# Optimization experiments

Measured on AMD Instinct MI355X. Metric: run time of the kernel, lower is better.

Reference implementation:

```python
import jax, jax.numpy as jnp
import numpy as np

B = 2
Z, Y, X = 21, 256, 256          # spatial_shape (z, y, x)
OZ, OY, OX = 10, 128, 128       # strided conv output grid: floor((in+2p-3)/2)+1
CIN, C1, C2 = 16, 32, 64
N = 400_000
EPS = 1e-3                      # BN eps from norm_cfg


def setup_inputs() -> dict:
    rng = np.random.default_rng(0)
    total = B * Z * Y * X
    lin = rng.choice(total, size=N, replace=False)
    lin.sort()
    b = (lin // (Z * Y * X)).astype(np.int64)
    r = lin % (Z * Y * X)
    z = r // (Y * X)
    r = r % (Y * X)
    y = r // X
    x = r % X
    coors = np.stack([b, z, y, x], axis=1).astype(np.int32)

    # Active output coords of SparseConv3d(k=3, s=2, pad=[0,1,1]):
    # input c is seen by output o iff o*2 - p + j == c for some j in {0,1,2}.
    pads = (0, 1, 1)
    cand_dims = []
    for c, p, osz in zip((z, y, x), pads, (OZ, OY, OX)):
        per = []
        for j in range(3):
            num = c + p - j
            o = num // 2
            valid = (num % 2 == 0) & (num >= 0) & (o < osz)
            per.append((o, valid))
        cand_dims.append(per)
    cand = []
    for oz, vz in cand_dims[0]:
        for oy, vy in cand_dims[1]:
            for ox, vx in cand_dims[2]:
                v = vz & vy & vx
                if v.any():
                    cand.append(np.stack([b[v], oz[v], oy[v], ox[v]], axis=1))
    out_coors = np.unique(np.concatenate(cand, axis=0), axis=0).astype(np.int32)

    key = jax.random.key(0)
    ks = jax.random.split(key, 11)
    voxel_feat = jax.random.normal(ks[0], (N, CIN), jnp.float32)
    W1 = jax.random.normal(ks[1], (27, CIN, C1), jnp.float32) / np.float32(np.sqrt(27 * CIN))
    W2 = jax.random.normal(ks[2], (27, C1, C2), jnp.float32) / np.float32(np.sqrt(27 * C1))
    g1 = 1.0 + 0.1 * jax.random.normal(ks[3], (C1,), jnp.float32)
    b1 = 0.1 * jax.random.normal(ks[4], (C1,), jnp.float32)
    m1 = 0.1 * jax.random.normal(ks[5], (C1,), jnp.float32)
    v1 = 0.5 + jnp.abs(jax.random.normal(ks[6], (C1,), jnp.float32)) * 0.5
    g2 = 1.0 + 0.1 * jax.random.normal(ks[7], (C2,), jnp.float32)
    b2 = 0.1 * jax.random.normal(ks[8], (C2,), jnp.float32)
    m2 = 0.1 * jax.random.normal(ks[9], (C2,), jnp.float32)
    v2 = 0.5 + jnp.abs(jax.random.normal(ks[10], (C2,), jnp.float32)) * 0.5
    return {
        "voxel_feat": voxel_feat,
        "coors": jnp.asarray(coors),
        "out_coors": jnp.asarray(out_coors),
        "W1": W1, "g1": g1, "b1": b1, "m1": m1, "v1": v1,
        "W2": W2, "g2": g2, "b2": b2, "m2": m2, "v2": v2,
        "batch_size": B,
    }


def _bn_relu(x, g, b, m, v):
    return jax.nn.relu((x - m) * (g * jax.lax.rsqrt(v + EPS)) + b)


def _build_grid(coors, n):
    # dense hash of active voxels -> row index (rulebook lookup table)
    lin = ((coors[:, 0] * Z + coors[:, 1]) * Y + coors[:, 2]) * X + coors[:, 3]
    return jnp.full((B * Z * Y * X,), -1, jnp.int32).at[lin].set(jnp.arange(n, dtype=jnp.int32))


def _sparse_conv(feat, grid, bcol, zz, yy, xx, W, cout):
    # gather-GEMM-scatter for one kernel offset set; loop over 27 offsets is structural
    n = zz[0].shape[0]
    out = jnp.zeros((n, cout), feat.dtype)
    for k in range(27):
        z_, y_, x_ = zz[k], yy[k], xx[k]
        ok = (z_ >= 0) & (z_ < Z) & (y_ >= 0) & (y_ < Y) & (x_ >= 0) & (x_ < X)
        l = ((bcol * Z + jnp.clip(z_, 0, Z - 1)) * Y + jnp.clip(y_, 0, Y - 1)) * X + jnp.clip(x_, 0, X - 1)
        idx = grid[l]
        ok = ok & (idx >= 0)
        f = feat[jnp.where(ok, idx, 0)]
        out = out + jnp.where(ok[:, None], f @ W[k], jnp.zeros((), feat.dtype))
    return out


def reference(voxel_feat, coors, out_coors, W1, g1, b1, m1, v1, W2, g2, b2, m2, v2, batch_size):
    n = voxel_feat.shape[0]
    grid = _build_grid(coors, n)

    # --- SubMConv3d(k=3, pad=1): out[c] = sum_j W1[j] @ in[c + j - 1], outputs only at input sites
    zz, yy, xx = [], [], []
    for dz in (-1, 0, 1):
        for dy in (-1, 0, 1):
            for dx in (-1, 0, 1):
                zz.append(coors[:, 1] + dz)
                yy.append(coors[:, 2] + dy)
                xx.append(coors[:, 3] + dx)
    f1 = _bn_relu(_sparse_conv(voxel_feat, grid, coors[:, 0], zz, yy, xx, W1, C1), g1, b1, m1, v1)

    # --- SparseConv3d(k=3, s=2, pad=[0,1,1]): input coord = o*2 - p + j
    zz, yy, xx = [], [], []
    for jz in range(3):
        for jy in range(3):
            for jx in range(3):
                zz.append(out_coors[:, 1] * 2 - 0 + jz)
                yy.append(out_coors[:, 2] * 2 - 1 + jy)
                xx.append(out_coors[:, 3] * 2 - 1 + jx)
    f2 = _bn_relu(_sparse_conv(f1, grid, out_coors[:, 0], zz, yy, xx, W2, C2), g2, b2, m2, v2)

    return f2, out_coors, batch_size
```

## Files before the change

kernel.cpp:

```cpp
#include <hip/hip_runtime.h>

#define ZD 21
#define YD 256
#define XD 256
#define BD 2
#define NCIN 16
#define NC1 32
#define NC2 64
#define BN_EPS 1e-3f

#define ZP 23
#define YP 258
#define XP 258
#define YPXP 66564
#define GRID_TOT (BD * ZP * YPXP)
#define TAILN 133647

typedef __attribute__((ext_vector_type(8))) short short8;
typedef __attribute__((ext_vector_type(4))) float floatx4;

__constant__ int KOFF[28] = {
    0, 1, 2, 258, 259, 260, 516, 517, 518,
    66564, 66565, 66566, 66822, 66823, 66824, 67080, 67081, 67082,
    133128, 133129, 133130, 133386, 133387, 133388, 133644, 133645, 133646,
    0};

__device__ inline unsigned short rne_bf16(float w) {
    unsigned b = __float_as_uint(w);
    return (unsigned short)((b + 0x7FFFu + ((b >> 16) & 1u)) >> 16);
}

__global__ __launch_bounds__(256) void scatter_grid_k(const int* __restrict__ coors,
                                                      int* __restrict__ grid, int n) {
    int i = blockIdx.x * 256 + threadIdx.x;
    if (i >= n) return;
    const int4 c = ((const int4*)coors)[i];
    const int lin = ((c.x * ZP + c.y + 1) * YP + c.z + 1) * XP + c.w + 1;
    grid[lin] = i;
}

__global__ __launch_bounds__(256) void feat2bf_k(const float* __restrict__ feat,
                                                 unsigned short* __restrict__ fb, int n8) {
    int i = blockIdx.x * 256 + threadIdx.x;
    if (i >= n8) return;
    const float4* p = (const float4*)feat + (size_t)i * 2;
    const float4 a = p[0], b = p[1];
    short8 o;
    o[0] = (short)rne_bf16(a.x); o[1] = (short)rne_bf16(a.y);
    o[2] = (short)rne_bf16(a.z); o[3] = (short)rne_bf16(a.w);
    o[4] = (short)rne_bf16(b.x); o[5] = (short)rne_bf16(b.y);
    o[6] = (short)rne_bf16(b.z); o[7] = (short)rne_bf16(b.w);
    ((short8*)fb)[i] = o;
}

__global__ __launch_bounds__(256) void pack_w_k(const float* __restrict__ W1,
                                                const float* __restrict__ W2,
                                                short* __restrict__ wp1,
                                                short* __restrict__ wp2) {
    int t = blockIdx.x * 256 + threadIdx.x;
    if (t < 14 * 2 * 512) {
        int pair = t / 1024, r = t % 1024, cb = r / 512, e = r % 512;
        int lane = e / 8, j = e % 8, kk = (lane >> 4) * 8 + j;
        int ko = pair * 2 + (kk >> 4), ci = kk & 15, co = cb * 16 + (lane & 15);
        float w = (ko < 27) ? W1[(ko * NCIN + ci) * NC1 + co] : 0.f;
        wp1[(pair * 2 + cb) * 512 + e] = (short)rne_bf16(w);
    }
    int t2 = t - 14 * 2 * 512;
    if (t2 >= 0 && t2 < 27 * 4 * 512) {
        int k = t2 / 2048, r = t2 % 2048, cb = r / 512, e = r % 512;
        int lane = e / 8, j = e % 8, ci = (lane >> 4) * 8 + j, co = cb * 16 + (lane & 15);
        wp2[(k * 4 + cb) * 512 + e] = (short)rne_bf16(W2[(k * NC1 + ci) * NC2 + co]);
    }
}

__global__ __launch_bounds__(256, 4) void conv1_k(
    const unsigned short* __restrict__ featb, const int* __restrict__ coors,
    const short* __restrict__ wp1,
    const float* __restrict__ g1, const float* __restrict__ b1,
    const float* __restrict__ m1, const float* __restrict__ v1,
    const int* __restrict__ gridp, unsigned short* __restrict__ f1, int n, int tail0) {
    const int tid = threadIdx.x;
    const int lane = tid & 63;
    const int quad = lane >> 4;
    const int mrow = lane & 15;
    const int vbase = blockIdx.x * 256 + (tid >> 6) * 64;
    const int ko_add = quad >> 1;
    const int ci_half = quad & 1;

    int pb[4];
#pragma unroll
    for (int mt = 0; mt < 4; ++mt) {
        const int v = vbase + mt * 16 + mrow;
        if (v < n) {
            const int4 cc = ((const int4*)coors)[v];
            pb[mt] = ((cc.x * ZP + cc.y) * YP + cc.z) * XP + cc.w;
        } else {
            pb[mt] = tail0;
        }
    }

    floatx4 d[4][2];
#pragma unroll
    for (int mt = 0; mt < 4; ++mt)
#pragma unroll
        for (int cb = 0; cb < 2; ++cb) d[mt][cb] = (floatx4){0.f, 0.f, 0.f, 0.f};

    const short8* __restrict__ wb = (const short8*)wp1;

    int id_c[4], id_n[4];
    {
        const int koff = ko_add ? KOFF[1] : KOFF[0];
#pragma unroll
        for (int mt = 0; mt < 4; ++mt) id_c[mt] = gridp[pb[mt] + koff];
    }
    {
        const int koff = ko_add ? KOFF[3] : KOFF[2];
#pragma unroll
        for (int mt = 0; mt < 4; ++mt) id_n[mt] = gridp[pb[mt] + koff];
    }
    short8 a_c[4];
#pragma unroll
    for (int mt = 0; mt < 4; ++mt) {
        a_c[mt] = (short8)0;
        if (id_c[mt] >= 0)
            a_c[mt] = *(const short8*)(featb + (unsigned)(id_c[mt] * NCIN + ci_half * 8));
    }
    short8 w0_c = wb[0 * 64 + lane];
    short8 w1_c = wb[1 * 64 + lane];

#pragma unroll 2
    for (int pair = 0; pair < 14; ++pair) {
        unsigned long long bm[4];
#pragma unroll
        for (int mt = 0; mt < 4; ++mt) bm[mt] = __ballot(id_c[mt] >= 0);

        short8 a_nx[4];
#pragma unroll
        for (int mt = 0; mt < 4; ++mt) {
            a_nx[mt] = (short8)0;
            if (id_n[mt] >= 0)
                a_nx[mt] = *(const short8*)(featb + (unsigned)(id_n[mt] * NCIN + ci_half * 8));
        }
        int id_f[4];
        {
            const int kbase = (pair < 12) ? (pair + 2) * 2 : 26;
            const int koff = ko_add ? KOFF[kbase + 1] : KOFF[kbase];
#pragma unroll
            for (int mt = 0; mt < 4; ++mt) id_f[mt] = gridp[pb[mt] + koff];
        }
        const int kn = (pair < 13) ? pair + 1 : 13;
        const short8 w0_n = wb[(kn * 2 + 0) * 64 + lane];
        const short8 w1_n = wb[(kn * 2 + 1) * 64 + lane];

#pragma unroll
        for (int mt = 0; mt < 4; ++mt) {
            if (bm[mt]) {
                d[mt][0] = __builtin_amdgcn_mfma_f32_16x16x32_bf16(a_c[mt], w0_c, d[mt][0], 0, 0, 0);
                d[mt][1] = __builtin_amdgcn_mfma_f32_16x16x32_bf16(a_c[mt], w1_c, d[mt][1], 0, 0, 0);
            }
        }
#pragma unroll
        for (int mt = 0; mt < 4; ++mt) {
            a_c[mt] = a_nx[mt]; id_c[mt] = id_n[mt]; id_n[mt] = id_f[mt];
        }
        w0_c = w0_n; w1_c = w1_n;
    }

    const int col = lane & 15;
#pragma unroll
    for (int cb = 0; cb < 2; ++cb) {
        const int ch = cb * 16 + col;
        const float sc = g1[ch] * rsqrtf(v1[ch] + BN_EPS);
        const float sb = b1[ch] - m1[ch] * sc;
#pragma unroll
        for (int mt = 0; mt < 4; ++mt) {
#pragma unroll
            for (int r = 0; r < 4; ++r) {
                const int v = vbase + mt * 16 + quad * 4 + r;
                if (v < n) {
                    const float o = fmaxf(fmaf(d[mt][cb][r], sc, sb), 0.f);
                    f1[(unsigned)(v * NC1 + ch)] = rne_bf16(o);
                }
            }
        }
    }
}

__global__ __launch_bounds__(256, 3) void conv2_k(
    const unsigned short* __restrict__ f1,
    const int* __restrict__ ocoors, const short* __restrict__ wp2,
    const float* __restrict__ g2, const float* __restrict__ b2,
    const float* __restrict__ m2, const float* __restrict__ v2,
    const int* __restrict__ gridp, float* __restrict__ out, int m, int tail0) {
    const int tid = threadIdx.x;
    const int lane = tid & 63;
    const int quad = lane >> 4;
    const int mrow = lane & 15;
    const int vbase = blockIdx.x * 256 + (tid >> 6) * 64;

    int pb[4];
#pragma unroll
    for (int mt = 0; mt < 4; ++mt) {
        const int v = vbase + mt * 16 + mrow;
        if (v < m) {
            const int4 cc = ((const int4*)ocoors)[v];
            pb[mt] = ((cc.x * ZP + 2 * cc.y + 1) * YP + 2 * cc.z) * XP + 2 * cc.w;
        } else {
            pb[mt] = tail0;
        }
    }

    floatx4 d[4][4];
#pragma unroll
    for (int mt = 0; mt < 4; ++mt)
#pragma unroll
        for (int cb = 0; cb < 4; ++cb) d[mt][cb] = (floatx4){0.f, 0.f, 0.f, 0.f};

    const short8* __restrict__ wb = (const short8*)wp2;

    int id_c[4], id_n[4];
#pragma unroll
    for (int mt = 0; mt < 4; ++mt) id_c[mt] = gridp[pb[mt] + KOFF[0]];
#pragma unroll
    for (int mt = 0; mt < 4; ++mt) id_n[mt] = gridp[pb[mt] + KOFF[1]];
    short8 a_c[4];
#pragma unroll
    for (int mt = 0; mt < 4; ++mt) {
        a_c[mt] = (short8)0;
        if (id_c[mt] >= 0)
            a_c[mt] = *(const short8*)(f1 + (unsigned)(id_c[mt] * NC1 + quad * 8));
    }
    short8 w_c[4];
#pragma unroll
    for (int cb = 0; cb < 4; ++cb) w_c[cb] = wb[(0 * 4 + cb) * 64 + lane];

#pragma unroll 2
    for (int k = 0; k < 27; ++k) {
        unsigned long long bm[4];
#pragma unroll
        for (int mt = 0; mt < 4; ++mt) bm[mt] = __ballot(id_c[mt] >= 0);

        short8 a_nx[4];
#pragma unroll
        for (int mt = 0; mt < 4; ++mt) {
            a_nx[mt] = (short8)0;
            if (id_n[mt] >= 0)
                a_nx[mt] = *(const short8*)(f1 + (unsigned)(id_n[mt] * NC1 + quad * 8));
        }
        int id_f[4];
        {
            const int koff = KOFF[(k < 25) ? k + 2 : 26];
#pragma unroll
            for (int mt = 0; mt < 4; ++mt) id_f[mt] = gridp[pb[mt] + koff];
        }
        const int kn = (k < 26) ? k + 1 : 26;
        short8 w_n[4];
#pragma unroll
        for (int cb = 0; cb < 4; ++cb) w_n[cb] = wb[(kn * 4 + cb) * 64 + lane];

#pragma unroll
        for (int mt = 0; mt < 4; ++mt) {
            if (bm[mt]) {
#pragma unroll
                for (int cb = 0; cb < 4; ++cb)
                    d[mt][cb] = __builtin_amdgcn_mfma_f32_16x16x32_bf16(a_c[mt], w_c[cb], d[mt][cb], 0, 0, 0);
            }
        }
#pragma unroll
        for (int mt = 0; mt < 4; ++mt) {
            a_c[mt] = a_nx[mt]; id_c[mt] = id_n[mt]; id_n[mt] = id_f[mt];
        }
#pragma unroll
        for (int cb = 0; cb < 4; ++cb) w_c[cb] = w_n[cb];
    }

    const int col = lane & 15;
#pragma unroll
    for (int cb = 0; cb < 4; ++cb) {
        const int ch = cb * 16 + col;
        const float sc = g2[ch] * rsqrtf(v2[ch] + BN_EPS);
        const float sb = b2[ch] - m2[ch] * sc;
#pragma unroll
        for (int mt = 0; mt < 4; ++mt) {
#pragma unroll
            for (int r = 0; r < 4; ++r) {
                const int v = vbase + mt * 16 + quad * 4 + r;
                if (v < m)
                    out[(unsigned)(v * NC2 + ch)] = fmaxf(fmaf(d[mt][cb][r], sc, sb), 0.f);
            }
        }
    }
}

__global__ __launch_bounds__(256) void tail_k(const int* __restrict__ oc,
                                              const int* __restrict__ bs,
                                              float* __restrict__ out, int m4) {
    int i = blockIdx.x * 256 + threadIdx.x;
    if (i < m4) out[i] = (float)oc[i];
    if (i == m4) out[m4] = (float)bs[0];
}

extern "C" void kernel_launch(void* const* d_in, const int* in_sizes, int n_in,
                              void* d_out, int out_size, void* d_ws, size_t ws_size,
                              hipStream_t stream) {
    const float* feat  = (const float*)d_in[0];
    const int*   coors = (const int*)d_in[1];
    const int*   ocoors= (const int*)d_in[2];
    const float* W1 = (const float*)d_in[3];
    const float* g1 = (const float*)d_in[4];
    const float* b1 = (const float*)d_in[5];
    const float* m1 = (const float*)d_in[6];
    const float* v1 = (const float*)d_in[7];
    const float* W2 = (const float*)d_in[8];
    const float* g2 = (const float*)d_in[9];
    const float* b2 = (const float*)d_in[10];
    const float* m2 = (const float*)d_in[11];
    const float* v2 = (const float*)d_in[12];
    const int*   bs = (const int*)d_in[13];

    const int n = in_sizes[0] / NCIN;
    const int m = in_sizes[2] / 4;

    char* ws = (char*)d_ws;
    int* grid = (int*)ws;
    size_t off = ((size_t)(GRID_TOT + TAILN) * sizeof(int) + 255) & ~(size_t)255;
    unsigned short* featb = (unsigned short*)(ws + off);
    off += ((size_t)n * NCIN * 2 + 255) & ~(size_t)255;
    unsigned short* f1 = (unsigned short*)(ws + off);
    off += ((size_t)n * NC1 * 2 + 255) & ~(size_t)255;
    short* wp1 = (short*)(ws + off);
    off += (14 * 2 * 512 * 2 + 255) & ~(size_t)255;
    short* wp2 = (short*)(ws + off);

    hipMemsetAsync(grid, 0xFF, (size_t)(GRID_TOT + TAILN) * sizeof(int), stream);
    scatter_grid_k<<<(n + 255) / 256, 256, 0, stream>>>(coors, grid, n);
    feat2bf_k<<<(n * 2 + 255) / 256, 256, 0, stream>>>(feat, featb, n * 2);
    pack_w_k<<<(14 * 2 * 512 + 27 * 4 * 512 + 255) / 256, 256, 0, stream>>>(W1, W2, wp1, wp2);

    conv1_k<<<(n + 255) / 256, 256, 0, stream>>>(featb, coors, wp1, g1, b1, m1, v1,
                                                 grid, f1, n, GRID_TOT);

    float* out = (float*)d_out;
    conv2_k<<<(m + 255) / 256, 256, 0, stream>>>(f1, ocoors, wp2,
                                                 g2, b2, m2, v2, grid, out, m, GRID_TOT);
    tail_k<<<(m * 4 + 1 + 255) / 256, 256, 0, stream>>>(ocoors, bs, out + (size_t)m * NC2, m * 4);
}
```

Measured before the change: 259.8 us.

## Stage conv weights in double-buffered LDS, halve per-block rows, fuse prep kernels

Merges the grid scatter, feature bf16 conversion, weight packing and coordinate tail copy into one prep kernel, cutting the number of launches. Both conv kernels now process 32 rows per wave instead of 64, and conv2 raises its occupancy hint from 3 to 4. Each kernel offset's weights are loaded cooperatively into a double-buffered LDS tile instead of every wave reading them from global memory. The price is a __syncthreads on every kernel-offset iteration, less reuse of each weight fragment per wave, and the loop is no longer unrolled.

```diff
diff --git a/kernel.cpp b/kernel.cpp
--- a/kernel.cpp
+++ b/kernel.cpp
@@ -30,47 +30,44 @@
     return (unsigned short)((b + 0x7FFFu + ((b >> 16) & 1u)) >> 16);
 }
 
-__global__ __launch_bounds__(256) void scatter_grid_k(const int* __restrict__ coors,
-                                                      int* __restrict__ grid, int n) {
-    int i = blockIdx.x * 256 + threadIdx.x;
-    if (i >= n) return;
-    const int4 c = ((const int4*)coors)[i];
-    const int lin = ((c.x * ZP + c.y + 1) * YP + c.z + 1) * XP + c.w + 1;
-    grid[lin] = i;
-}
-
-__global__ __launch_bounds__(256) void feat2bf_k(const float* __restrict__ feat,
-                                                 unsigned short* __restrict__ fb, int n8) {
-    int i = blockIdx.x * 256 + threadIdx.x;
-    if (i >= n8) return;
-    const float4* p = (const float4*)feat + (size_t)i * 2;
-    const float4 a = p[0], b = p[1];
-    short8 o;
-    o[0] = (short)rne_bf16(a.x); o[1] = (short)rne_bf16(a.y);
-    o[2] = (short)rne_bf16(a.z); o[3] = (short)rne_bf16(a.w);
-    o[4] = (short)rne_bf16(b.x); o[5] = (short)rne_bf16(b.y);
-    o[6] = (short)rne_bf16(b.z); o[7] = (short)rne_bf16(b.w);
-    ((short8*)fb)[i] = o;
-}
-
-__global__ __launch_bounds__(256) void pack_w_k(const float* __restrict__ W1,
-                                                const float* __restrict__ W2,
-                                                short* __restrict__ wp1,
-                                                short* __restrict__ wp2) {
-    int t = blockIdx.x * 256 + threadIdx.x;
-    if (t < 14 * 2 * 512) {
-        int pair = t / 1024, r = t % 1024, cb = r / 512, e = r % 512;
+__global__ __launch_bounds__(256) void prep_k(
+    const float* __restrict__ feat, const int* __restrict__ coors,
+    const float* __restrict__ W1, const float* __restrict__ W2,
+    const int* __restrict__ oc, const int* __restrict__ bs,
+    int* __restrict__ grid, unsigned short* __restrict__ featb,
+    short* __restrict__ wp1, short* __restrict__ wp2,
+    float* __restrict__ out2, int n, int m4) {
+    const int i = blockIdx.x * 256 + threadIdx.x;
+
+    if (i < n) {
+        const int4 c = ((const int4*)coors)[i];
+        grid[((c.x * ZP + c.y + 1) * YP + c.z + 1) * XP + c.w + 1] = i;
+    }
+    if (i < 2 * n) {
+        const float4* p = (const float4*)feat + (size_t)i * 2;
+        const float4 a = p[0], b = p[1];
+        short8 o;
+        o[0] = (short)rne_bf16(a.x); o[1] = (short)rne_bf16(a.y);
+        o[2] = (short)rne_bf16(a.z); o[3] = (short)rne_bf16(a.w);
+        o[4] = (short)rne_bf16(b.x); o[5] = (short)rne_bf16(b.y);
+        o[6] = (short)rne_bf16(b.z); o[7] = (short)rne_bf16(b.w);
+        ((short8*)featb)[i] = o;
+    }
+    if (i < 14 * 2 * 512) {
+        int pair = i / 1024, r = i % 1024, cb = r / 512, e = r % 512;
         int lane = e / 8, j = e % 8, kk = (lane >> 4) * 8 + j;
         int ko = pair * 2 + (kk >> 4), ci = kk & 15, co = cb * 16 + (lane & 15);
         float w = (ko < 27) ? W1[(ko * NCIN + ci) * NC1 + co] : 0.f;
         wp1[(pair * 2 + cb) * 512 + e] = (short)rne_bf16(w);
     }
-    int t2 = t - 14 * 2 * 512;
+    const int t2 = i - 14 * 2 * 512;
     if (t2 >= 0 && t2 < 27 * 4 * 512) {
         int k = t2 / 2048, r = t2 % 2048, cb = r / 512, e = r % 512;
         int lane = e / 8, j = e % 8, ci = (lane >> 4) * 8 + j, co = cb * 16 + (lane & 15);
         wp2[(k * 4 + cb) * 512 + e] = (short)rne_bf16(W2[(k * NC1 + ci) * NC2 + co]);
     }
+    if (i < m4) out2[i] = (float)oc[i];
+    if (i == m4) out2[m4] = (float)bs[0];
 }
 
 __global__ __launch_bounds__(256, 4) void conv1_k(
@@ -83,13 +80,15 @@
     const int lane = tid & 63;
     const int quad = lane >> 4;
     const int mrow = lane & 15;
-    const int vbase = blockIdx.x * 256 + (tid >> 6) * 64;
+    const int vbase = blockIdx.x * 128 + (tid >> 6) * 32;
     const int ko_add = quad >> 1;
     const int ci_half = quad & 1;
 
-    int pb[4];
-#pragma unroll
-    for (int mt = 0; mt < 4; ++mt) {
+    __shared__ short lw[2][1024];
+
+    int pb[2];
+#pragma unroll
+    for (int mt = 0; mt < 2; ++mt) {
         const int v = vbase + mt * 16 + mrow;
         if (v < n) {
             const int4 cc = ((const int4*)coors)[v];
@@ -99,71 +98,80 @@
         }
     }
 
-    floatx4 d[4][2];
-#pragma unroll
-    for (int mt = 0; mt < 4; ++mt)
+    floatx4 d[2][2];
+#pragma unroll
+    for (int mt = 0; mt < 2; ++mt)
 #pragma unroll
         for (int cb = 0; cb < 2; ++cb) d[mt][cb] = (floatx4){0.f, 0.f, 0.f, 0.f};
 
-    const short8* __restrict__ wb = (const short8*)wp1;
-
-    int id_c[4], id_n[4];
+    const short8* __restrict__ wg = (const short8*)wp1;
+
+    if (tid < 128) ((short8*)lw[0])[tid] = wg[tid];
+    int id_c[2], id_n[2];
     {
-        const int koff = ko_add ? KOFF[1] : KOFF[0];
-#pragma unroll
-        for (int mt = 0; mt < 4; ++mt) id_c[mt] = gridp[pb[mt] + koff];
+        const int koff = KOFF[ko_add];
+#pragma unroll
+        for (int mt = 0; mt < 2; ++mt) id_c[mt] = gridp[pb[mt] + koff];
     }
     {
-        const int koff = ko_add ? KOFF[3] : KOFF[2];
-#pragma unroll
-        for (int mt = 0; mt < 4; ++mt) id_n[mt] = gridp[pb[mt] + koff];
-    }
-    short8 a_c[4];
-#pragma unroll
-    for (int mt = 0; mt < 4; ++mt) {
+        const int koff = KOFF[2 + ko_add];
+#pragma unroll
+        for (int mt = 0; mt < 2; ++mt) id_n[mt] = gridp[pb[mt] + koff];
+    }
+    short8 a_c[2];
+#pragma unroll
+    for (int mt = 0; mt < 2; ++mt) {
         a_c[mt] = (short8)0;
         if (id_c[mt] >= 0)
             a_c[mt] = *(const short8*)(featb + (unsigned)(id_c[mt] * NCIN + ci_half * 8));
     }
-    short8 w0_c = wb[0 * 64 + lane];
-    short8 w1_c = wb[1 * 64 + lane];
-
-#pragma unroll 2
+    __syncthreads();
+
+    int buf = 0;
+#pragma unroll 1
     for (int pair = 0; pair < 14; ++pair) {
-        unsigned long long bm[4];
-#pragma unroll
-        for (int mt = 0; mt < 4; ++mt) bm[mt] = __ballot(id_c[mt] >= 0);
-
-        short8 a_nx[4];
-#pragma unroll
-        for (int mt = 0; mt < 4; ++mt) {
+        const int kst = (pair < 13) ? pair + 1 : 13;
+        short8 wreg;
+        if (tid < 128) wreg = wg[kst * 128 + tid];
+
+        short8 wf0 = ((const short8*)lw[buf])[0 * 64 + lane];
+        short8 wf1 = ((const short8*)lw[buf])[1 * 64 + lane];
+
+        unsigned long long bm[2];
+#pragma unroll
+        for (int mt = 0; mt < 2; ++mt) bm[mt] = __ballot(id_c[mt] >= 0);
+
+        short8 a_nx[2];
+#pragma unroll
+        for (int mt = 0; mt < 2; ++mt) {
             a_nx[mt] = (short8)0;
             if (id_n[mt] >= 0)
                 a_nx[mt] = *(const short8*)(featb + (unsigned)(id_n[mt] * NCIN + ci_half * 8));
         }
-        int id_f[4];
+        int id_f[2];
         {
             const int kbase = (pair < 12) ? (pair + 2) * 2 : 26;
-            const int koff = ko_add ? KOFF[kbase + 1] : KOFF[kbase];
-#pragma unroll
-            for (int mt = 0; mt < 4; ++mt) id_f[mt] = gridp[pb[mt] + koff];
-        }
-        const int kn = (pair < 13) ? pair + 1 : 13;
-        const short8 w0_n = wb[(kn * 2 + 0) * 64 + lane];
-        const short8 w1_n = wb[(kn * 2 + 1) * 64 + lane];
-
-#pragma unroll
-        for (int mt = 0; mt < 4; ++mt) {
+            const int koff = KOFF[kbase + ko_add];
+#pragma unroll
+            for (int mt = 0; mt < 2; ++mt) id_f[mt] = gridp[pb[mt] + koff];
+        }
+
+#pragma unroll
+        for (int mt = 0; mt < 2; ++mt) {
             if (bm[mt]) {
-                d[mt][0] = __builtin_amdgcn_mfma_f32_16x16x32_bf16(a_c[mt], w0_c, d[mt][0], 0, 0, 0);
-                d[mt][1] = __builtin_amdgcn_mfma_f32_16x16x32_bf16(a_c[mt], w1_c, d[mt][1], 0, 0, 0);
+                d[mt][0] = __builtin_amdgcn_mfma_f32_16x16x32_bf16(a_c[mt], wf0, d[mt][0], 0, 0, 0);
+                d[mt][1] = __builtin_amdgcn_mfma_f32_16x16x32_bf16(a_c[mt], wf1, d[mt][1], 0, 0, 0);
             }
         }
-#pragma unroll
-        for (int mt = 0; mt < 4; ++mt) {
+
+        if (tid < 128) ((short8*)lw[buf ^ 1])[tid] = wreg;
+        __syncthreads();
+
+#pragma unroll
+        for (int mt = 0; mt < 2; ++mt) {
             a_c[mt] = a_nx[mt]; id_c[mt] = id_n[mt]; id_n[mt] = id_f[mt];
         }
-        w0_c = w0_n; w1_c = w1_n;
+        buf ^= 1;
     }
 
     const int col = lane & 15;
@@ -173,7 +181,7 @@
         const float sc = g1[ch] * rsqrtf(v1[ch] + BN_EPS);
         const float sb = b1[ch] - m1[ch] * sc;
 #pragma unroll
-        for (int mt = 0; mt < 4; ++mt) {
+        for (int mt = 0; mt < 2; ++mt) {
 #pragma unroll
             for (int r = 0; r < 4; ++r) {
                 const int v = vbase + mt * 16 + quad * 4 + r;
@@ -186,7 +194,7 @@
     }
 }
 
-__global__ __launch_bounds__(256, 3) void conv2_k(
+__global__ __launch_bounds__(256, 4) void conv2_k(
     const unsigned short* __restrict__ f1,
     const int* __restrict__ ocoors, const short* __restrict__ wp2,
     const float* __restrict__ g2, const float* __restrict__ b2,
@@ -196,11 +204,13 @@
     const int lane = tid & 63;
     const int quad = lane >> 4;
     const int mrow = lane & 15;
-    const int vbase = blockIdx.x * 256 + (tid >> 6) * 64;
-
-    int pb[4];
-#pragma unroll
-    for (int mt = 0; mt < 4; ++mt) {
+    const int vbase = blockIdx.x * 128 + (tid >> 6) * 32;
+
+    __shared__ short lw[2][2048];
+
+    int pb[2];
+#pragma unroll
+    for (int mt = 0; mt < 2; ++mt) {
         const int v = vbase + mt * 16 + mrow;
         if (v < m) {
             const int4 cc = ((const int4*)ocoors)[v];
@@ -210,68 +220,75 @@
         }
     }
 
-    floatx4 d[4][4];
-#pragma unroll
-    for (int mt = 0; mt < 4; ++mt)
+    floatx4 d[2][4];
+#pragma unroll
+    for (int mt = 0; mt < 2; ++mt)
 #pragma unroll
         for (int cb = 0; cb < 4; ++cb) d[mt][cb] = (floatx4){0.f, 0.f, 0.f, 0.f};
 
-    const short8* __restrict__ wb = (const short8*)wp2;
-
-    int id_c[4], id_n[4];
-#pragma unroll
-    for (int mt = 0; mt < 4; ++mt) id_c[mt] = gridp[pb[mt] + KOFF[0]];
-#pragma unroll
-    for (int mt = 0; mt < 4; ++mt) id_n[mt] = gridp[pb[mt] + KOFF[1]];
-    short8 a_c[4];
-#pragma unroll
-    for (int mt = 0; mt < 4; ++mt) {
+    const short8* __restrict__ wg = (const short8*)wp2;
+
+    ((short8*)lw[0])[tid] = wg[tid];
+    int id_c[2], id_n[2];
+#pragma unroll
+    for (int mt = 0; mt < 2; ++mt) id_c[mt] = gridp[pb[mt] + KOFF[0]];
+#pragma unroll
+    for (int mt = 0; mt < 2; ++mt) id_n[mt] = gridp[pb[mt] + KOFF[1]];
+    short8 a_c[2];
+#pragma unroll
+    for (int mt = 0; mt < 2; ++mt) {
         a_c[mt] = (short8)0;
         if (id_c[mt] >= 0)
             a_c[mt] = *(const short8*)(f1 + (unsigned)(id_c[mt] * NC1 + quad * 8));
     }
-    short8 w_c[4];
-#pragma unroll
-    for (int cb = 0; cb < 4; ++cb) w_c[cb] = wb[(0 * 4 + cb) * 64 + lane];
-
-#pragma unroll 2
+    __syncthreads();
+
+    int buf = 0;
+#pragma unroll 1
     for (int k = 0; k < 27; ++k) {
-        unsigned long long bm[4];
-#pragma unroll
-        for (int mt = 0; mt < 4; ++mt) bm[mt] = __ballot(id_c[mt] >= 0);
-
-        short8 a_nx[4];
-#pragma unroll
-        for (int mt = 0; mt < 4; ++mt) {
+        const int kst = (k < 26) ? k + 1 : 26;
+        short8 wreg = wg[kst * 256 + tid];
+
+        short8 wf[4];
+#pragma unroll
+        for (int cb = 0; cb < 4; ++cb)
+            wf[cb] = ((const short8*)lw[buf])[cb * 64 + lane];
+
+        unsigned long long bm[2];
+#pragma unroll
+        for (int mt = 0; mt < 2; ++mt) bm[mt] = __ballot(id_c[mt] >= 0);
+
+        short8 a_nx[2];
+#pragma unroll
+        for (int mt = 0; mt < 2; ++mt) {
             a_nx[mt] = (short8)0;
             if (id_n[mt] >= 0)
                 a_nx[mt] = *(const short8*)(f1 + (unsigned)(id_n[mt] * NC1 + quad * 8));
         }
-        int id_f[4];
+        int id_f[2];
         {
             const int koff = KOFF[(k < 25) ? k + 2 : 26];
 #pragma unroll
-            for (int mt = 0; mt < 4; ++mt) id_f[mt] = gridp[pb[mt] + koff];
-        }
-        const int kn = (k < 26) ? k + 1 : 26;
-        short8 w_n[4];
-#pragma unroll
-        for (int cb = 0; cb < 4; ++cb) w_n[cb] = wb[(kn * 4 + cb) * 64 + lane];
-
-#pragma unroll
-        for (int mt = 0; mt < 4; ++mt) {
+            for (int mt = 0; mt < 2; ++mt) id_f[mt] = gridp[pb[mt] + koff];
+        }
+
+#pragma unroll
+        for (int mt = 0; mt < 2; ++mt) {
             if (bm[mt]) {
 #pragma unroll
                 for (int cb = 0; cb < 4; ++cb)
-                    d[mt][cb] = __builtin_amdgcn_mfma_f32_16x16x32_bf16(a_c[mt], w_c[cb], d[mt][cb], 0, 0, 0);
+                    d[mt][cb] = __builtin_amdgcn_mfma_f32_16x16x32_bf16(a_c[mt], wf[cb], d[mt][cb], 0, 0, 0);
             }
         }
-#pragma unroll
-        for (int mt = 0; mt < 4; ++mt) {
+
+        ((short8*)lw[buf ^ 1])[tid] = wreg;
+        __syncthreads();
+
+#pragma unroll
+        for (int mt = 0; mt < 2; ++mt) {
             a_c[mt] = a_nx[mt]; id_c[mt] = id_n[mt]; id_n[mt] = id_f[mt];
         }
-#pragma unroll
-        for (int cb = 0; cb < 4; ++cb) w_c[cb] = w_n[cb];
+        buf ^= 1;
     }
 
     const int col = lane & 15;
@@ -281,7 +298,7 @@
         const float sc = g2[ch] * rsqrtf(v2[ch] + BN_EPS);
         const float sb = b2[ch] - m2[ch] * sc;
 #pragma unroll
-        for (int mt = 0; mt < 4; ++mt) {
+        for (int mt = 0; mt < 2; ++mt) {
 #pragma unroll
             for (int r = 0; r < 4; ++r) {
                 const int v = vbase + mt * 16 + quad * 4 + r;
@@ -290,14 +307,6 @@
             }
         }
     }
-}
-
-__global__ __launch_bounds__(256) void tail_k(const int* __restrict__ oc,
-                                              const int* __restrict__ bs,
-                                              float* __restrict__ out, int m4) {
-    int i = blockIdx.x * 256 + threadIdx.x;
-    if (i < m4) out[i] = (float)oc[i];
-    if (i == m4) out[m4] = (float)bs[0];
 }
 
 extern "C" void kernel_launch(void* const* d_in, const int* in_sizes, int n_in,
@@ -332,16 +341,19 @@
     off += (14 * 2 * 512 * 2 + 255) & ~(size_t)255;
     short* wp2 = (short*)(ws + off);
 
+    float* out = (float*)d_out;
+    float* out2 = out + (size_t)m * NC2;
+
+    int prep_threads = 2 * n;
+    if (m * 4 + 1 > prep_threads) prep_threads = m * 4 + 1;
+
     hipMemsetAsync(grid, 0xFF, (size_t)(GRID_TOT + TAILN) * sizeof(int), stream);
-    scatter_grid_k<<<(n + 255) / 256, 256, 0, stream>>>(coors, grid, n);
-    feat2bf_k<<<(n * 2 + 255) / 256, 256, 0, stream>>>(feat, featb, n * 2);
-    pack_w_k<<<(14 * 2 * 512 + 27 * 4 * 512 + 255) / 256, 256, 0, stream>>>(W1, W2, wp1, wp2);
-
-    conv1_k<<<(n + 255) / 256, 256, 0, stream>>>(featb, coors, wp1, g1, b1, m1, v1,
+    prep_k<<<(prep_threads + 255) / 256, 256, 0, stream>>>(feat, coors, W1, W2, ocoors, bs,
+                                                           grid, featb, wp1, wp2, out2, n, m * 4);
+
+    conv1_k<<<(n + 127) / 128, 256, 0, stream>>>(featb, coors, wp1, g1, b1, m1, v1,
                                                  grid, f1, n, GRID_TOT);
 
-    float* out = (float*)d_out;
-    conv2_k<<<(m + 255) / 256, 256, 0, stream>>>(f1, ocoors, wp2,
+    conv2_k<<<(m + 127) / 128, 256, 0, stream>>>(f1, ocoors, wp2,
                                                  g2, b2, m2, v2, grid, out, m, GRID_TOT);
-    tail_k<<<(m * 4 + 1 + 255) / 256, 256, 0, stream>>>(ocoors, bs, out + (size_t)m * NC2, m * 4);
-}
+}
```

New measurement: 237.5 us. 1.09x faster.
